# Kernel optimization log

Hardware: AMD Instinct MI355X
Metric: run time of the kernel (lower is better)

## Reference

```python
import jax, jax.numpy as jnp
import numpy as np

NGRAM = 4
PAD = 0
N_LAYERS = sum(range(1, NGRAM + 1)) - 1  # 9; blocks_size = 10


def setup_inputs() -> dict:
    B, L, D, V = 8, 2048, 256, 256
    rng = np.random.default_rng(0)
    lens = rng.integers(L // 2, L + 1, size=B)
    pos = np.arange(L)
    seq = rng.integers(1, V, size=(B, L))
    seq = np.where(pos[None, :] < lens[:, None], seq, PAD)
    # per-layer block sizes: (size,offset) combos of GBST, sizes [2,2,3,3,3,4,4,4,4]
    sizes = [n for n in range(1, NGRAM + 1) for _ in range(n)][1:]
    gid = np.zeros((B, N_LAYERS, L), dtype=np.int64)
    for li, s in enumerate(sizes):
        g = pos // s + 1  # sorted contiguous group ids starting at 1
        gid[:, li, :] = np.where(pos[None, :] < lens[:, None], g[None, :], PAD)

    key = jax.random.key(0)
    ks = jax.random.split(key, 8)
    emb = jax.random.normal(ks[0], (V, D), jnp.float32) * 0.02
    conv_w = jax.random.normal(ks[1], (D, 1, NGRAM), jnp.float32) * 0.3      # depthwise Conv1d weight [out,1,k]
    conv_b = jax.random.normal(ks[2], (D,), jnp.float32) * 0.01
    proj_w = jax.random.normal(ks[3], (D, D), jnp.float32) / np.sqrt(D)      # 1x1 conv as [out,in]
    proj_b = jax.random.normal(ks[4], (D,), jnp.float32) * 0.01
    score_w = jax.random.normal(ks[5], (D,), jnp.float32) / np.sqrt(D)       # Linear(D,1)
    score_b = jnp.zeros((), jnp.float32)
    ff_w = jax.random.normal(ks[6], (D, D), jnp.float32) / np.sqrt(D)        # Linear(D,D) weight [out,in]
    ff_b = jax.random.normal(ks[7], (D,), jnp.float32) * 0.01
    return {
        "sequence": jnp.asarray(seq, jnp.int64) if jax.config.jax_enable_x64 else jnp.asarray(seq, jnp.int32),
        "group_id": jnp.asarray(gid, jnp.int64) if jax.config.jax_enable_x64 else jnp.asarray(gid, jnp.int32),
        "emb": emb, "conv_w": conv_w, "conv_b": conv_b,
        "proj_w": proj_w, "proj_b": proj_b,
        "score_w": score_w, "score_b": score_b,
        "ff_w": ff_w, "ff_b": ff_b,
    }


def _pool_one(xb, gb):
    """Per-(batch,layer) scatter_mean + broadcast back. xb:[L,D], gb:[L]."""
    L = gb.shape[0]
    mask = gb == PAD
    xm = jnp.where(mask[:, None], 0.0, xb)          # zero padded positions
    pad_g = jnp.max(gb) + 1                         # pad positions -> extra trailing group
    g = jnp.where(mask, pad_g, gb) - 1              # 0-based group ids
    sums = jax.ops.segment_sum(xm, g, num_segments=L)
    cnts = jax.ops.segment_sum(jnp.ones((L,), xb.dtype), g, num_segments=L)
    means = sums / jnp.maximum(cnts, 1.0)[:, None]
    # group ids are sorted-contiguous, so repeat_interleave(bincount) == gather
    return means[g]


def reference(sequence, group_id, emb, conv_w, conv_b, proj_w, proj_b,
              score_w, score_b, ff_w, ff_b):
    B, L = sequence.shape
    D = emb.shape[1]
    # NormalizedEmbedding: lookup * sqrt(d_model)
    x = emb[sequence] * jnp.sqrt(jnp.asarray(D, emb.dtype))          # [B,L,D]
    xp = jnp.pad(x, ((0, 0), (0, NGRAM - 1), (0, 0)))                # pad seq end
    xc = xp.transpose(0, 2, 1)                                       # [B,D,L+k-1]
    xc = jax.lax.conv_general_dilated(
        xc, conv_w, window_strides=(1,), padding='VALID',
        feature_group_count=D, dimension_numbers=('NCH', 'OIH', 'NCH'))
    xc = xc + conv_b[None, :, None]
    xc = jnp.einsum('ed,bdl->bel', proj_w, xc) + proj_b[None, :, None]
    x = xc.transpose(0, 2, 1)                                        # [B,L,D]
    seq_mask = sequence == PAD
    x = jnp.where(seq_mask[..., None], 0.0, x)

    # layers 1..9 are computed on a detached copy in the original
    xd = jax.lax.stop_gradient(x)
    pooled = jax.vmap(jax.vmap(_pool_one, in_axes=(None, 0)),
                      in_axes=(0, 0))(xd, group_id)                  # [B,9,L,D]

    block_reps = jnp.concatenate([x[:, None], pooled], axis=1)       # [B,10,L,D]
    block_reps = block_reps.transpose(0, 2, 1, 3)                    # [B,L,10,D]

    scores = jnp.einsum('blsd,d->bls', block_reps, score_w) + score_b
    blocks_mask = jnp.concatenate([sequence[:, None], group_id], axis=1)
    blocks_mask = blocks_mask.transpose(0, 2, 1) == PAD              # [B,L,10]
    neg = -jnp.finfo(scores.dtype).max
    scores = jnp.where(blocks_mask, neg, scores)
    scores = jax.nn.softmax(scores, axis=2)

    out = jnp.einsum('blsd,bls->bld', block_reps, scores)            # [B,L,D]
    out = out + jax.nn.relu(out @ ff_w.T + ff_b)
    return out
```

## Files before the change

### kernel.cpp

```cpp
#include <hip/hip_runtime.h>
#include <math.h>


#define D_ 256
#define M_ 24
#define BPB 86
#define LSTR 264

typedef __attribute__((ext_vector_type(8))) short bf16x8;
typedef __attribute__((ext_vector_type(4))) float f32x4;

__device__ __forceinline__ ushort f2bf(float f) {
    union { float f; unsigned u; } v; v.f = f;
    unsigned r = v.u + 0x7fffu + ((v.u >> 16) & 1u);
    return (ushort)(r >> 16);
}
__device__ __forceinline__ float bf2f(ushort h) {
    union { unsigned u; float f; } v; v.u = ((unsigned)h) << 16;
    return v.f;
}

#define LDB4(v0, v1, v2, v3, W, K8) do { \
    const ushort* bp_ = (W) + ((size_t)((K8) * 16 + w * 4) * 64 + ln) * 8; \
    v0 = *(const bf16x8*)(bp_); \
    v1 = *(const bf16x8*)(bp_ + 512); \
    v2 = *(const bf16x8*)(bp_ + 1024); \
    v3 = *(const bf16x8*)(bp_ + 1536); \
} while (0)

#define MFMA8(ACC, K8, v0, v1, v2, v3) do { \
    bf16x8 a0_ = *(const bf16x8*)&x_lds[lr][(K8) * 32 + koff]; \
    bf16x8 a1_ = *(const bf16x8*)&x_lds[16 + lr][(K8) * 32 + koff]; \
    ACC[0][0] = __builtin_amdgcn_mfma_f32_16x16x32_bf16(a0_, v0, ACC[0][0], 0, 0, 0); \
    ACC[1][0] = __builtin_amdgcn_mfma_f32_16x16x32_bf16(a1_, v0, ACC[1][0], 0, 0, 0); \
    ACC[0][1] = __builtin_amdgcn_mfma_f32_16x16x32_bf16(a0_, v1, ACC[0][1], 0, 0, 0); \
    ACC[1][1] = __builtin_amdgcn_mfma_f32_16x16x32_bf16(a1_, v1, ACC[1][1], 0, 0, 0); \
    ACC[0][2] = __builtin_amdgcn_mfma_f32_16x16x32_bf16(a0_, v2, ACC[0][2], 0, 0, 0); \
    ACC[1][2] = __builtin_amdgcn_mfma_f32_16x16x32_bf16(a1_, v2, ACC[1][2], 0, 0, 0); \
    ACC[0][3] = __builtin_amdgcn_mfma_f32_16x16x32_bf16(a0_, v3, ACC[0][3], 0, 0, 0); \
    ACC[1][3] = __builtin_amdgcn_mfma_f32_16x16x32_bf16(a1_, v3, ACC[1][3], 0, 0, 0); \
} while (0)

#define SBAR __builtin_amdgcn_sched_barrier(0)

__global__ __launch_bounds__(256) void k_prep(
    const float* __restrict__ pw, const float* __restrict__ fw,
    ushort* __restrict__ wqp, ushort* __restrict__ wqf)
{
    int i = blockIdx.x * 256 + threadIdx.x;
    int j  = i & 7;
    int ln = (i >> 3) & 63;
    int nb = (i >> 9) & 15;
    int k8 = i >> 13;
    int er = nb * 16 + (ln & 15);
    int k  = k8 * 32 + (ln >> 4) * 8 + j;
    wqp[i] = f2bf(pw[er * D_ + k]);
    wqf[i] = f2bf(fw[er * D_ + k]);
}

__global__ __launch_bounds__(256, 4) void k_main(
    const int* __restrict__ seq, const float* __restrict__ emb,
    const float* __restrict__ conv_w, const float* __restrict__ conv_b,
    const ushort* __restrict__ wqp, const float* __restrict__ proj_b,
    const float* __restrict__ score_w,
    const ushort* __restrict__ wqf, const float* __restrict__ ff_b,
    float* __restrict__ out, int L)
{
    __shared__ ushort x_lds[32][LSTR];
    __shared__ ushort x2[M_][LSTR];
    __shared__ float xsred[4][M_];
    __shared__ float wts[4][12][4];
    const int b  = blockIdx.x / BPB;
    const int l0 = (blockIdx.x % BPB) * M_;
    const int t  = threadIdx.x;
    const int w  = t >> 6, ln = t & 63;
    const int lr = ln & 15, q = ln >> 4;
    const int koff = q * 8;

    int tok[M_ + 3];
    {
        const int* seqp = seq + (size_t)b * L + l0;
        #pragma unroll
        for (int r = 0; r < M_ + 3; ++r) {
            int tv = -1;
            if (l0 + r < L) tv = __builtin_amdgcn_readfirstlane(seqp[r]);
            tok[r] = tv;
        }
    }
    unsigned vmask = 0;
    #pragma unroll
    for (int r = 0; r < M_; ++r) vmask |= (tok[r] > 0) ? (1u << r) : 0u;

    bf16x8 s00, s01, s02, s03, s10, s11, s12, s13, s20, s21, s22, s23;
    LDB4(s00, s01, s02, s03, wqp, 0);
    LDB4(s10, s11, s12, s13, wqp, 1);
    LDB4(s20, s21, s22, s23, wqp, 2);
    SBAR;

    {
        int zr = 24 + (t >> 5), zc = (t & 31) * 8;
        *(uint4*)&x_lds[zr][zc] = make_uint4(0, 0, 0, 0);
    }

    {
        const int h = t >> 7;
        const int ch0 = (t & 127) * 2;
        float4 wa = *(const float4*)(conv_w + ch0 * 4);
        float4 wb = *(const float4*)(conv_w + ch0 * 4 + 4);
        wa.x *= 16.f; wa.y *= 16.f; wa.z *= 16.f; wa.w *= 16.f;
        wb.x *= 16.f; wb.y *= 16.f; wb.z *= 16.f; wb.w *= 16.f;
        const float cba = conv_b[ch0], cbb = conv_b[ch0 + 1];
        #define CONV_HALF(BASE) do { \
            float2 er[15]; \
            _Pragma("unroll") \
            for (int r = 0; r < 15; ++r) { \
                int sn = tok[(BASE) + r]; \
                float2 e; e.x = 0.f; e.y = 0.f; \
                if (sn >= 0) e = *(const float2*)(emb + (size_t)sn * D_ + ch0); \
                er[r] = e; \
            } \
            _Pragma("unroll") \
            for (int r = 0; r < 12; ++r) { \
                float cx = fmaf(wa.x, er[r].x, fmaf(wa.y, er[r+1].x, \
                           fmaf(wa.z, er[r+2].x, fmaf(wa.w, er[r+3].x, cba)))); \
                float cy = fmaf(wb.x, er[r].y, fmaf(wb.y, er[r+1].y, \
                           fmaf(wb.z, er[r+2].y, fmaf(wb.w, er[r+3].y, cbb)))); \
                *(unsigned*)&x_lds[(BASE) + r][ch0] = \
                    (unsigned)f2bf(cx) | ((unsigned)f2bf(cy) << 16); \
            } \
        } while (0)
        if (h == 0) { CONV_HALF(0); } else { CONV_HALF(12); }
        #undef CONV_HALF
    }
    __syncthreads();

    f32x4 acc[2][4];
    #pragma unroll
    for (int s = 0; s < 2; ++s)
        #pragma unroll
        for (int n = 0; n < 4; ++n) acc[s][n] = (f32x4){0.f, 0.f, 0.f, 0.f};
    MFMA8(acc, 0, s00, s01, s02, s03); LDB4(s00, s01, s02, s03, wqp, 3); SBAR;
    MFMA8(acc, 1, s10, s11, s12, s13); LDB4(s10, s11, s12, s13, wqp, 4); SBAR;
    MFMA8(acc, 2, s20, s21, s22, s23); LDB4(s20, s21, s22, s23, wqp, 5); SBAR;
    MFMA8(acc, 3, s00, s01, s02, s03); LDB4(s00, s01, s02, s03, wqp, 6); SBAR;
    MFMA8(acc, 4, s10, s11, s12, s13); LDB4(s10, s11, s12, s13, wqp, 7); SBAR;
    MFMA8(acc, 5, s20, s21, s22, s23);
    MFMA8(acc, 6, s00, s01, s02, s03);
    MFMA8(acc, 7, s10, s11, s12, s13);

    {
        float xsp[8] = {0,0,0,0,0,0,0,0};
        #pragma unroll
        for (int n = 0; n < 4; ++n) {
            int e = w * 64 + n * 16 + lr;
            float pb = proj_b[e], sw = score_w[e];
            #pragma unroll
            for (int s = 0; s < 2; ++s) {
                #pragma unroll
                for (int r = 0; r < 4; ++r) {
                    int row = s * 16 + q * 4 + r;
                    if (row < M_) {
                        float v = ((vmask >> row) & 1u) ? acc[s][n][r] + pb : 0.f;
                        x2[row][e] = f2bf(v);
                        xsp[s * 4 + r] = fmaf(v, sw, xsp[s * 4 + r]);
                    }
                }
            }
        }
        #pragma unroll
        for (int off = 1; off < 16; off <<= 1) {
            #pragma unroll
            for (int i = 0; i < 8; ++i) xsp[i] += __shfl_xor(xsp[i], off, 64);
        }
        if (lr == 0) {
            #pragma unroll
            for (int r = 0; r < 4; ++r) xsred[w][q * 4 + r] = xsp[r];
            if (q < 2) {
                #pragma unroll
                for (int r = 0; r < 4; ++r) xsred[w][16 + q * 4 + r] = xsp[4 + r];
            }
        }
    }
    __syncthreads();

    LDB4(s00, s01, s02, s03, wqf, 0);
    LDB4(s10, s11, s12, s13, wqf, 1);
    LDB4(s20, s21, s22, s23, wqf, 2);
    SBAR;

    if (ln < 12) {
        const int p = (w >> 1) * 12 + ln;
        if (!((vmask >> p) & 1u)) {
            wts[w][ln][0] = wts[w][ln][1] = wts[w][ln][2] = wts[w][ln][3] = 0.f;
        } else {
            #define XS(i) (xsred[0][i] + xsred[1][i] + xsred[2][i] + xsred[3][i])
            float s0 = XS(p);
            int r2 = p & ~1;
            float c2 = (float)__popc((vmask >> r2) & 3u);
            float m2 = (XS(r2) + XS(r2 + 1)) / c2;
            int r3 = p - (p % 3);
            float c3 = (float)__popc((vmask >> r3) & 7u);
            float m3 = (XS(r3) + XS(r3 + 1) + XS(r3 + 2)) / c3;
            int r4 = p & ~3;
            float c4 = (float)__popc((vmask >> r4) & 15u);
            float m4 = (XS(r4) + XS(r4 + 1) + XS(r4 + 2) + XS(r4 + 3)) / c4;
            float mx = fmaxf(fmaxf(s0, m2), fmaxf(m3, m4));
            float q0 = __expf(s0 - mx), q2 = __expf(m2 - mx);
            float q3 = __expf(m3 - mx), q4 = __expf(m4 - mx);
            float iZ = 1.f / (q0 + 2.f * q2 + 3.f * q3 + 4.f * q4);
            wts[w][ln][0] = q0 * iZ;
            wts[w][ln][1] = 2.f * q2 * iZ / c2;
            wts[w][ln][2] = 3.f * q3 * iZ / c3;
            wts[w][ln][3] = 4.f * q4 * iZ / c4;
            #undef XS
        }
    }
    asm volatile("s_waitcnt lgkmcnt(0)" ::: "memory");
    SBAR;

    {
        const int tile = t >> 7;
        const int r0 = tile * 12;
        const int ch0 = (t & 127) * 2;
        float2 xr[12];
        #pragma unroll
        for (int p = 0; p < 12; ++p) {
            unsigned v = *(const unsigned*)&x2[r0 + p][ch0];
            xr[p].x = bf2f((ushort)(v & 0xffff));
            xr[p].y = bf2f((ushort)(v >> 16));
        }
        float s2x[6], s2y[6], s3x[4], s3y[4], s4x[3], s4y[3];
        #pragma unroll
        for (int j = 0; j < 6; ++j) {
            s2x[j] = xr[2*j].x + xr[2*j+1].x;
            s2y[j] = xr[2*j].y + xr[2*j+1].y;
        }
        #pragma unroll
        for (int j = 0; j < 4; ++j) {
            s3x[j] = xr[3*j].x + xr[3*j+1].x + xr[3*j+2].x;
            s3y[j] = xr[3*j].y + xr[3*j+1].y + xr[3*j+2].y;
        }
        #pragma unroll
        for (int j = 0; j < 3; ++j) {
            s4x[j] = xr[4*j].x + xr[4*j+1].x + xr[4*j+2].x + xr[4*j+3].x;
            s4y[j] = xr[4*j].y + xr[4*j+1].y + xr[4*j+2].y + xr[4*j+3].y;
        }
        #pragma unroll
        for (int p = 0; p < 12; ++p) {
            float4 wv = *(const float4*)&wts[w][p][0];
            float ox = wv.x*xr[p].x + wv.y*s2x[p>>1] + wv.z*s3x[p/3] + wv.w*s4x[p>>2];
            float oy = wv.x*xr[p].y + wv.y*s2y[p>>1] + wv.z*s3y[p/3] + wv.w*s4y[p>>2];
            *(unsigned*)&x_lds[r0 + p][ch0] =
                (unsigned)f2bf(ox) | ((unsigned)f2bf(oy) << 16);
        }
    }
    __syncthreads();

    f32x4 ffa[2][4];
    #pragma unroll
    for (int s = 0; s < 2; ++s)
        #pragma unroll
        for (int n = 0; n < 4; ++n) ffa[s][n] = (f32x4){0.f, 0.f, 0.f, 0.f};
    MFMA8(ffa, 0, s00, s01, s02, s03); LDB4(s00, s01, s02, s03, wqf, 3); SBAR;
    MFMA8(ffa, 1, s10, s11, s12, s13); LDB4(s10, s11, s12, s13, wqf, 4); SBAR;
    MFMA8(ffa, 2, s20, s21, s22, s23); LDB4(s20, s21, s22, s23, wqf, 5); SBAR;
    MFMA8(ffa, 3, s00, s01, s02, s03); LDB4(s00, s01, s02, s03, wqf, 6); SBAR;
    MFMA8(ffa, 4, s10, s11, s12, s13); LDB4(s10, s11, s12, s13, wqf, 7); SBAR;
    MFMA8(ffa, 5, s20, s21, s22, s23);
    MFMA8(ffa, 6, s00, s01, s02, s03);
    MFMA8(ffa, 7, s10, s11, s12, s13);

    #pragma unroll
    for (int n = 0; n < 4; ++n) {
        int e = w * 64 + n * 16 + lr;
        float fb = ff_b[e];
        #pragma unroll
        for (int s = 0; s < 2; ++s) {
            #pragma unroll
            for (int r = 0; r < 4; ++r) {
                int row = s * 16 + q * 4 + r;
                if (row < M_) {
                    int l = l0 + row;
                    if (l < L) {
                        float o = bf2f(x_lds[row][e]);
                        out[((size_t)b * L + l) * D_ + e]
                            = o + fmaxf(ffa[s][n][r] + fb, 0.f);
                    }
                }
            }
        }
    }
}

extern "C" void kernel_launch(void* const* d_in, const int* in_sizes, int n_in,
                              void* d_out, int out_size, void* d_ws, size_t ws_size,
                              hipStream_t stream) {
    const int*   seq     = (const int*)d_in[0];
    const float* emb     = (const float*)d_in[2];
    const float* conv_w  = (const float*)d_in[3];
    const float* conv_b  = (const float*)d_in[4];
    const float* proj_w  = (const float*)d_in[5];
    const float* proj_b  = (const float*)d_in[6];
    const float* score_w = (const float*)d_in[7];
    const float* ff_w    = (const float*)d_in[9];
    const float* ff_b    = (const float*)d_in[10];
    float* out = (float*)d_out;

    const int L = 2048;
    const int B = in_sizes[0] / L;

    ushort* wqp = (ushort*)d_ws;
    ushort* wqf = wqp + D_ * D_;

    k_prep<<<D_ * D_ / 256, 256, 0, stream>>>(proj_w, ff_w, wqp, wqf);
    k_main<<<B * BPB, 256, 0, stream>>>(seq, emb, conv_w, conv_b, wqp, proj_b,
                                        score_w, wqf, ff_b, out, L);
}
```

Baseline: 28.53 us.

## Double row tile to 48 with 512-thread blocks and halved per-wave MFMA width

Each block now handles 48 sequence rows with 8 waves instead of 24 rows with 4 waves. Each wave covers 32 output columns over three 16-row MFMA tiles, which removes the zero-padded rows the 24-row tile needed (32 rows computed for 24 used) and halves per-wave weight-fragment loads. The token mask is built with a ballot instead of a per-thread token array, and the group score sums use wave shuffles instead of repeated LDS reads. The trade-offs are half as many blocks (344 instead of 688), more LDS per block, and larger blocks that may lower occupancy.

Measured after the change: 28.72 us. About the same (+0.7%).

```diff
diff --git a/kernel.cpp b/kernel.cpp
--- a/kernel.cpp
+++ b/kernel.cpp
@@ -3,8 +3,8 @@
 
 
 #define D_ 256
-#define M_ 24
-#define BPB 86
+#define M_ 48
+#define BPB 43
 #define LSTR 264
 
 typedef __attribute__((ext_vector_type(8))) short bf16x8;
@@ -20,25 +20,22 @@
     return v.f;
 }
 
-#define LDB4(v0, v1, v2, v3, W, K8) do { \
-    const ushort* bp_ = (W) + ((size_t)((K8) * 16 + w * 4) * 64 + ln) * 8; \
+#define LDB2(v0, v1, W, K8) do { \
+    const ushort* bp_ = (W) + ((size_t)((K8) * 16 + w * 2) * 64 + ln) * 8; \
     v0 = *(const bf16x8*)(bp_); \
     v1 = *(const bf16x8*)(bp_ + 512); \
-    v2 = *(const bf16x8*)(bp_ + 1024); \
-    v3 = *(const bf16x8*)(bp_ + 1536); \
 } while (0)
 
-#define MFMA8(ACC, K8, v0, v1, v2, v3) do { \
+#define MFMA6(ACC, K8, v0, v1) do { \
     bf16x8 a0_ = *(const bf16x8*)&x_lds[lr][(K8) * 32 + koff]; \
     bf16x8 a1_ = *(const bf16x8*)&x_lds[16 + lr][(K8) * 32 + koff]; \
+    bf16x8 a2_ = *(const bf16x8*)&x_lds[32 + lr][(K8) * 32 + koff]; \
     ACC[0][0] = __builtin_amdgcn_mfma_f32_16x16x32_bf16(a0_, v0, ACC[0][0], 0, 0, 0); \
     ACC[1][0] = __builtin_amdgcn_mfma_f32_16x16x32_bf16(a1_, v0, ACC[1][0], 0, 0, 0); \
+    ACC[2][0] = __builtin_amdgcn_mfma_f32_16x16x32_bf16(a2_, v0, ACC[2][0], 0, 0, 0); \
     ACC[0][1] = __builtin_amdgcn_mfma_f32_16x16x32_bf16(a0_, v1, ACC[0][1], 0, 0, 0); \
     ACC[1][1] = __builtin_amdgcn_mfma_f32_16x16x32_bf16(a1_, v1, ACC[1][1], 0, 0, 0); \
-    ACC[0][2] = __builtin_amdgcn_mfma_f32_16x16x32_bf16(a0_, v2, ACC[0][2], 0, 0, 0); \
-    ACC[1][2] = __builtin_amdgcn_mfma_f32_16x16x32_bf16(a1_, v2, ACC[1][2], 0, 0, 0); \
-    ACC[0][3] = __builtin_amdgcn_mfma_f32_16x16x32_bf16(a0_, v3, ACC[0][3], 0, 0, 0); \
-    ACC[1][3] = __builtin_amdgcn_mfma_f32_16x16x32_bf16(a1_, v3, ACC[1][3], 0, 0, 0); \
+    ACC[2][1] = __builtin_amdgcn_mfma_f32_16x16x32_bf16(a2_, v1, ACC[2][1], 0, 0, 0); \
 } while (0)
 
 #define SBAR __builtin_amdgcn_sched_barrier(0)
@@ -58,7 +55,7 @@
     wqf[i] = f2bf(fw[er * D_ + k]);
 }
 
-__global__ __launch_bounds__(256, 4) void k_main(
+__global__ __launch_bounds__(512, 4) void k_main(
     const int* __restrict__ seq, const float* __restrict__ emb,
     const float* __restrict__ conv_w, const float* __restrict__ conv_b,
     const ushort* __restrict__ wqp, const float* __restrict__ proj_b,
@@ -66,58 +63,50 @@
     const ushort* __restrict__ wqf, const float* __restrict__ ff_b,
     float* __restrict__ out, int L)
 {
-    __shared__ ushort x_lds[32][LSTR];
+    __shared__ ushort x_lds[M_][LSTR];
     __shared__ ushort x2[M_][LSTR];
-    __shared__ float xsred[4][M_];
-    __shared__ float wts[4][12][4];
+    __shared__ float xsred[8][M_];
+    __shared__ float wts[8][12][4];
     const int b  = blockIdx.x / BPB;
     const int l0 = (blockIdx.x % BPB) * M_;
     const int t  = threadIdx.x;
     const int w  = t >> 6, ln = t & 63;
     const int lr = ln & 15, q = ln >> 4;
     const int koff = q * 8;
-
-    int tok[M_ + 3];
+    const int g   = t >> 7;
+    const int ch0 = (t & 127) * 2;
+
+    const int* seqp = seq + (size_t)b * L + l0;
+
+    unsigned long long vmask;
     {
-        const int* seqp = seq + (size_t)b * L + l0;
-        #pragma unroll
-        for (int r = 0; r < M_ + 3; ++r) {
-            int tv = -1;
-            if (l0 + r < L) tv = __builtin_amdgcn_readfirstlane(seqp[r]);
-            tok[r] = tv;
-        }
-    }
-    unsigned vmask = 0;
-    #pragma unroll
-    for (int r = 0; r < M_; ++r) vmask |= (tok[r] > 0) ? (1u << r) : 0u;
-
-    bf16x8 s00, s01, s02, s03, s10, s11, s12, s13, s20, s21, s22, s23;
-    LDB4(s00, s01, s02, s03, wqp, 0);
-    LDB4(s10, s11, s12, s13, wqp, 1);
-    LDB4(s20, s21, s22, s23, wqp, 2);
+        int sv = (ln < M_ && l0 + ln < L) ? seqp[ln] : 0;
+        vmask = __ballot(sv > 0);
+    }
+
+    bf16x8 s00, s01, s10, s11, s20, s21, s30, s31;
+    LDB2(s00, s01, wqp, 0);
+    LDB2(s10, s11, wqp, 1);
+    LDB2(s20, s21, wqp, 2);
+    LDB2(s30, s31, wqp, 3);
     SBAR;
 
     {
-        int zr = 24 + (t >> 5), zc = (t & 31) * 8;
-        *(uint4*)&x_lds[zr][zc] = make_uint4(0, 0, 0, 0);
-    }
-
-    {
-        const int h = t >> 7;
-        const int ch0 = (t & 127) * 2;
         float4 wa = *(const float4*)(conv_w + ch0 * 4);
         float4 wb = *(const float4*)(conv_w + ch0 * 4 + 4);
         wa.x *= 16.f; wa.y *= 16.f; wa.z *= 16.f; wa.w *= 16.f;
         wb.x *= 16.f; wb.y *= 16.f; wb.z *= 16.f; wb.w *= 16.f;
         const float cba = conv_b[ch0], cbb = conv_b[ch0 + 1];
-        #define CONV_HALF(BASE) do { \
+        #define CONV_GROUP(BASE) do { \
             float2 er[15]; \
             _Pragma("unroll") \
             for (int r = 0; r < 15; ++r) { \
-                int sn = tok[(BASE) + r]; \
-                float2 e; e.x = 0.f; e.y = 0.f; \
-                if (sn >= 0) e = *(const float2*)(emb + (size_t)sn * D_ + ch0); \
-                er[r] = e; \
+                float2 e_; e_.x = 0.f; e_.y = 0.f; \
+                if (l0 + (BASE) + r < L) { \
+                    int sn_ = __builtin_amdgcn_readfirstlane(seqp[(BASE) + r]); \
+                    e_ = *(const float2*)(emb + (size_t)sn_ * D_ + ch0); \
+                } \
+                er[r] = e_; \
             } \
             _Pragma("unroll") \
             for (int r = 0; r < 12; ++r) { \
@@ -129,99 +118,104 @@
                     (unsigned)f2bf(cx) | ((unsigned)f2bf(cy) << 16); \
             } \
         } while (0)
-        if (h == 0) { CONV_HALF(0); } else { CONV_HALF(12); }
-        #undef CONV_HALF
+        if      (g == 0) { CONV_GROUP(0);  }
+        else if (g == 1) { CONV_GROUP(12); }
+        else if (g == 2) { CONV_GROUP(24); }
+        else             { CONV_GROUP(36); }
+        #undef CONV_GROUP
     }
     __syncthreads();
 
-    f32x4 acc[2][4];
+    f32x4 acc[3][2];
     #pragma unroll
-    for (int s = 0; s < 2; ++s)
-        #pragma unroll
-        for (int n = 0; n < 4; ++n) acc[s][n] = (f32x4){0.f, 0.f, 0.f, 0.f};
-    MFMA8(acc, 0, s00, s01, s02, s03); LDB4(s00, s01, s02, s03, wqp, 3); SBAR;
-    MFMA8(acc, 1, s10, s11, s12, s13); LDB4(s10, s11, s12, s13, wqp, 4); SBAR;
-    MFMA8(acc, 2, s20, s21, s22, s23); LDB4(s20, s21, s22, s23, wqp, 5); SBAR;
-    MFMA8(acc, 3, s00, s01, s02, s03); LDB4(s00, s01, s02, s03, wqp, 6); SBAR;
-    MFMA8(acc, 4, s10, s11, s12, s13); LDB4(s10, s11, s12, s13, wqp, 7); SBAR;
-    MFMA8(acc, 5, s20, s21, s22, s23);
-    MFMA8(acc, 6, s00, s01, s02, s03);
-    MFMA8(acc, 7, s10, s11, s12, s13);
+    for (int s = 0; s < 3; ++s)
+        #pragma unroll
+        for (int n = 0; n < 2; ++n) acc[s][n] = (f32x4){0.f, 0.f, 0.f, 0.f};
+    MFMA6(acc, 0, s00, s01); LDB2(s00, s01, wqp, 4); SBAR;
+    MFMA6(acc, 1, s10, s11); LDB2(s10, s11, wqp, 5); SBAR;
+    MFMA6(acc, 2, s20, s21); LDB2(s20, s21, wqp, 6); SBAR;
+    MFMA6(acc, 3, s30, s31); LDB2(s30, s31, wqp, 7); SBAR;
+    MFMA6(acc, 4, s00, s01);
+    MFMA6(acc, 5, s10, s11);
+    MFMA6(acc, 6, s20, s21);
+    MFMA6(acc, 7, s30, s31);
 
     {
-        float xsp[8] = {0,0,0,0,0,0,0,0};
-        #pragma unroll
-        for (int n = 0; n < 4; ++n) {
-            int e = w * 64 + n * 16 + lr;
+        float xsp[12];
+        #pragma unroll
+        for (int i = 0; i < 12; ++i) xsp[i] = 0.f;
+        #pragma unroll
+        for (int n = 0; n < 2; ++n) {
+            int e = w * 32 + n * 16 + lr;
             float pb = proj_b[e], sw = score_w[e];
             #pragma unroll
-            for (int s = 0; s < 2; ++s) {
+            for (int s = 0; s < 3; ++s) {
                 #pragma unroll
                 for (int r = 0; r < 4; ++r) {
                     int row = s * 16 + q * 4 + r;
-                    if (row < M_) {
-                        float v = ((vmask >> row) & 1u) ? acc[s][n][r] + pb : 0.f;
-                        x2[row][e] = f2bf(v);
-                        xsp[s * 4 + r] = fmaf(v, sw, xsp[s * 4 + r]);
-                    }
+                    float v = ((vmask >> row) & 1ull) ? acc[s][n][r] + pb : 0.f;
+                    x2[row][e] = f2bf(v);
+                    xsp[s * 4 + r] = fmaf(v, sw, xsp[s * 4 + r]);
                 }
             }
         }
         #pragma unroll
         for (int off = 1; off < 16; off <<= 1) {
             #pragma unroll
-            for (int i = 0; i < 8; ++i) xsp[i] += __shfl_xor(xsp[i], off, 64);
+            for (int i = 0; i < 12; ++i) xsp[i] += __shfl_xor(xsp[i], off, 64);
         }
         if (lr == 0) {
             #pragma unroll
-            for (int r = 0; r < 4; ++r) xsred[w][q * 4 + r] = xsp[r];
-            if (q < 2) {
+            for (int s = 0; s < 3; ++s)
                 #pragma unroll
-                for (int r = 0; r < 4; ++r) xsred[w][16 + q * 4 + r] = xsp[4 + r];
-            }
+                for (int r = 0; r < 4; ++r)
+                    xsred[w][s * 16 + q * 4 + r] = xsp[s * 4 + r];
         }
     }
     __syncthreads();
 
-    LDB4(s00, s01, s02, s03, wqf, 0);
-    LDB4(s10, s11, s12, s13, wqf, 1);
-    LDB4(s20, s21, s22, s23, wqf, 2);
+    LDB2(s00, s01, wqf, 0);
+    LDB2(s10, s11, wqf, 1);
+    LDB2(s20, s21, wqf, 2);
+    LDB2(s30, s31, wqf, 3);
     SBAR;
 
     if (ln < 12) {
         const int p = (w >> 1) * 12 + ln;
-        if (!((vmask >> p) & 1u)) {
+        float xt = xsred[0][p] + xsred[1][p] + xsred[2][p] + xsred[3][p]
+                 + xsred[4][p] + xsred[5][p] + xsred[6][p] + xsred[7][p];
+        int i2 = ln & ~1;
+        float s2 = __shfl(xt, i2, 64) + __shfl(xt, i2 + 1, 64);
+        int i3 = ln - (ln % 3);
+        float s3 = __shfl(xt, i3, 64) + __shfl(xt, i3 + 1, 64)
+                 + __shfl(xt, i3 + 2, 64);
+        int i4 = ln & ~3;
+        float s4 = __shfl(xt, i4, 64) + __shfl(xt, i4 + 1, 64)
+                 + __shfl(xt, i4 + 2, 64) + __shfl(xt, i4 + 3, 64);
+        if (!((vmask >> p) & 1ull)) {
             wts[w][ln][0] = wts[w][ln][1] = wts[w][ln][2] = wts[w][ln][3] = 0.f;
         } else {
-            #define XS(i) (xsred[0][i] + xsred[1][i] + xsred[2][i] + xsred[3][i])
-            float s0 = XS(p);
-            int r2 = p & ~1;
-            float c2 = (float)__popc((vmask >> r2) & 3u);
-            float m2 = (XS(r2) + XS(r2 + 1)) / c2;
+            int r2 = p & ~1, r4 = p & ~3;
             int r3 = p - (p % 3);
-            float c3 = (float)__popc((vmask >> r3) & 7u);
-            float m3 = (XS(r3) + XS(r3 + 1) + XS(r3 + 2)) / c3;
-            int r4 = p & ~3;
-            float c4 = (float)__popc((vmask >> r4) & 15u);
-            float m4 = (XS(r4) + XS(r4 + 1) + XS(r4 + 2) + XS(r4 + 3)) / c4;
-            float mx = fmaxf(fmaxf(s0, m2), fmaxf(m3, m4));
-            float q0 = __expf(s0 - mx), q2 = __expf(m2 - mx);
+            float c2 = (float)__popcll((vmask >> r2) & 3ull);
+            float c3 = (float)__popcll((vmask >> r3) & 7ull);
+            float c4 = (float)__popcll((vmask >> r4) & 15ull);
+            float m2 = s2 / c2, m3 = s3 / c3, m4 = s4 / c4;
+            float mx = fmaxf(fmaxf(xt, m2), fmaxf(m3, m4));
+            float q0 = __expf(xt - mx), q2 = __expf(m2 - mx);
             float q3 = __expf(m3 - mx), q4 = __expf(m4 - mx);
             float iZ = 1.f / (q0 + 2.f * q2 + 3.f * q3 + 4.f * q4);
             wts[w][ln][0] = q0 * iZ;
             wts[w][ln][1] = 2.f * q2 * iZ / c2;
             wts[w][ln][2] = 3.f * q3 * iZ / c3;
             wts[w][ln][3] = 4.f * q4 * iZ / c4;
-            #undef XS
         }
     }
     asm volatile("s_waitcnt lgkmcnt(0)" ::: "memory");
     SBAR;
 
     {
-        const int tile = t >> 7;
-        const int r0 = tile * 12;
-        const int ch0 = (t & 127) * 2;
+        const int r0 = g * 12;
         float2 xr[12];
         #pragma unroll
         for (int p = 0; p < 12; ++p) {
@@ -256,36 +250,34 @@
     }
     __syncthreads();
 
-    f32x4 ffa[2][4];
+    f32x4 ffa[3][2];
     #pragma unroll
-    for (int s = 0; s < 2; ++s)
-        #pragma unroll
-        for (int n = 0; n < 4; ++n) ffa[s][n] = (f32x4){0.f, 0.f, 0.f, 0.f};
-    MFMA8(ffa, 0, s00, s01, s02, s03); LDB4(s00, s01, s02, s03, wqf, 3); SBAR;
-    MFMA8(ffa, 1, s10, s11, s12, s13); LDB4(s10, s11, s12, s13, wqf, 4); SBAR;
-    MFMA8(ffa, 2, s20, s21, s22, s23); LDB4(s20, s21, s22, s23, wqf, 5); SBAR;
-    MFMA8(ffa, 3, s00, s01, s02, s03); LDB4(s00, s01, s02, s03, wqf, 6); SBAR;
-    MFMA8(ffa, 4, s10, s11, s12, s13); LDB4(s10, s11, s12, s13, wqf, 7); SBAR;
-    MFMA8(ffa, 5, s20, s21, s22, s23);
-    MFMA8(ffa, 6, s00, s01, s02, s03);
-    MFMA8(ffa, 7, s10, s11, s12, s13);
+    for (int s = 0; s < 3; ++s)
+        #pragma unroll
+        for (int n = 0; n < 2; ++n) ffa[s][n] = (f32x4){0.f, 0.f, 0.f, 0.f};
+    MFMA6(ffa, 0, s00, s01); LDB2(s00, s01, wqf, 4); SBAR;
+    MFMA6(ffa, 1, s10, s11); LDB2(s10, s11, wqf, 5); SBAR;
+    MFMA6(ffa, 2, s20, s21); LDB2(s20, s21, wqf, 6); SBAR;
+    MFMA6(ffa, 3, s30, s31); LDB2(s30, s31, wqf, 7); SBAR;
+    MFMA6(ffa, 4, s00, s01);
+    MFMA6(ffa, 5, s10, s11);
+    MFMA6(ffa, 6, s20, s21);
+    MFMA6(ffa, 7, s30, s31);
 
     #pragma unroll
-    for (int n = 0; n < 4; ++n) {
-        int e = w * 64 + n * 16 + lr;
+    for (int n = 0; n < 2; ++n) {
+        int e = w * 32 + n * 16 + lr;
         float fb = ff_b[e];
         #pragma unroll
-        for (int s = 0; s < 2; ++s) {
+        for (int s = 0; s < 3; ++s) {
             #pragma unroll
             for (int r = 0; r < 4; ++r) {
                 int row = s * 16 + q * 4 + r;
-                if (row < M_) {
-                    int l = l0 + row;
-                    if (l < L) {
-                        float o = bf2f(x_lds[row][e]);
-                        out[((size_t)b * L + l) * D_ + e]
-                            = o + fmaxf(ffa[s][n][r] + fb, 0.f);
-                    }
+                int l = l0 + row;
+                if (l < L) {
+                    float o = bf2f(x_lds[row][e]);
+                    out[((size_t)b * L + l) * D_ + e]
+                        = o + fmaxf(ffa[s][n][r] + fb, 0.f);
                 }
             }
         }
@@ -313,6 +305,6 @@
     ushort* wqf = wqp + D_ * D_;
 
     k_prep<<<D_ * D_ / 256, 256, 0, stream>>>(proj_w, ff_w, wqp, wqf);
-    k_main<<<B * BPB, 256, 0, stream>>>(seq, emb, conv_w, conv_b, wqp, proj_b,
+    k_main<<<B * BPB, 512, 0, stream>>>(seq, emb, conv_w, conv_b, wqp, proj_b,
                                         score_w, wqf, ff_b, out, L);
 }
```
